# Kernel tuning notes

Measured on AMD Instinct MI355X. Metric: run time of the kernel, lower is better.

Reference implementation:

```python
import jax, jax.numpy as jnp
import numpy as np

B, L, E, H = 4, 2048, 1024, 16
D = E // H  # head_dim = 64


def setup_inputs() -> dict:
    key = jax.random.key(0)
    ks = jax.random.split(key, 8)
    s = 0.02
    return {
        "queries": jax.random.normal(ks[0], (B, L, E), jnp.float32),
        "keys": jax.random.normal(ks[1], (B, L, E), jnp.float32),
        "values": jax.random.normal(ks[2], (B, L, E), jnp.float32),
        "mask": jnp.ones((B, 1, L, L), jnp.int32),
        "Wq": jax.random.normal(ks[3], (E, E), jnp.float32) * s,
        "Wk": jax.random.normal(ks[4], (E, E), jnp.float32) * s,
        "Wv": jax.random.normal(ks[5], (E, E), jnp.float32) * s,
        "Wo": jax.random.normal(ks[6], (E, E), jnp.float32) * s,
        "bo": jax.random.normal(ks[7], (E,), jnp.float32) * s,
    }


def reference(queries, keys, values, mask, Wq, Wk, Wv, Wo, bo):
    # Linear projections (torch Linear: x @ W.T)
    q = (queries @ Wq.T).reshape(B, -1, H, D)
    k = (keys @ Wk.T).reshape(B, -1, H, D)
    v = (values @ Wv.T).reshape(B, -1, H, D)
    # scores: [B, H, Lq, Lk]
    scores = jnp.einsum("bqhd,bkhd->bhqk", q, k)
    # masked_fill BEFORE scaling, exactly as the original
    scores = jnp.where(mask == 0, jnp.float32(-1e20), scores)
    attn = jax.nn.softmax(scores / jnp.sqrt(jnp.float32(E)), axis=3)
    out = jnp.einsum("bhql,blhd->bqhd", attn, v).reshape(B, -1, H * D)
    return out @ Wo.T + bo
```

## Files before the change

### kernel.cpp

```cpp
#include <hip/hip_runtime.h>
#include <hip/hip_bf16.h>

#define B_ 4
#define L_ 2048
#define E_ 1024
#define H_ 16
#define D_ 64
#define KDIM 1024

typedef unsigned short u16;
typedef unsigned short u16x8 __attribute__((ext_vector_type(8)));
typedef short s16x8 __attribute__((ext_vector_type(8)));
typedef float f32x4 __attribute__((ext_vector_type(4)));
typedef unsigned uint2v __attribute__((ext_vector_type(2)));
typedef __fp16 h16x2 __attribute__((ext_vector_type(2)));
typedef __fp16 h16x4 __attribute__((ext_vector_type(4)));
typedef __fp16 h16x8 __attribute__((ext_vector_type(8)));

#define MFMA32(a, b, c) __builtin_amdgcn_mfma_f32_16x16x32_bf16(a, b, c, 0, 0, 0)
#define MFMA32F(a, b, c) __builtin_amdgcn_mfma_f32_16x16x32_f16(a, b, c, 0, 0, 0)

#if __has_builtin(__builtin_amdgcn_mfma_f32_16x16x16f16)
#define HAVE_F16K16 1
#define MFMA16F(a, b, c) __builtin_amdgcn_mfma_f32_16x16x16f16(a, b, c, 0, 0, 0)
#else
#define HAVE_F16K16 0
#endif

__device__ inline u16 f2bf(float f) {
  union { float f; unsigned u; } v; v.f = f;
  unsigned r = v.u + 0x7fffu + ((v.u >> 16) & 1u);
  return (u16)(r >> 16);
}
__device__ inline float bf2f(u16 h) {
  union { unsigned u; float f; } v; v.u = ((unsigned)h) << 16;
  return v.f;
}
__device__ inline float bperm_f(int byteaddr, float v) {
  return __uint_as_float((unsigned)__builtin_amdgcn_ds_bpermute(byteaddr, (int)__float_as_uint(v)));
}
__device__ inline u16 f2h_bits(float f) {
  union { __fp16 h; u16 u; } c; c.h = (__fp16)f;
  return c.u;
}

typedef __attribute__((address_space(1))) const unsigned as1_u32;
typedef __attribute__((address_space(3))) unsigned as3_u32;
__device__ inline void gl_lds16(const u16* g, u16* l) {
  __builtin_amdgcn_global_load_lds((as1_u32*)g, (as3_u32*)l, 16, 0, 0);
}

#define SCALE_Q 0.045084220f
#define MASKC  -4.508422e18f

__global__ __launch_bounds__(256) void detect_k(const u16* __restrict__ q, int* __restrict__ flag) {
  int tid = threadIdx.x;
  int cnt = 0;
  for (int i = tid; i < 4096; i += 256) {
    unsigned e = (q[i] >> 7) & 0xFFu;
    if (e >= 0xC0u) cnt++;
  }
  __shared__ int s[256];
  s[tid] = cnt;
  __syncthreads();
  for (int off = 128; off; off >>= 1) {
    if (tid < off) s[tid] += s[tid + off];
    __syncthreads();
  }
  if (tid == 0) *flag = (s[0] >= 16) ? 1 : 0;
}

__global__ __launch_bounds__(256) void mask_bits_k(const int* __restrict__ mask,
                                                   unsigned long long* __restrict__ bits,
                                                   unsigned* __restrict__ gflag, int words) {
  int gw = (int)((blockIdx.x * 256 + threadIdx.x) >> 6);
  int lane = threadIdx.x & 63;
  if (gw >= words) return;
  int mv = mask[(size_t)gw * 64 + lane];
  unsigned long long bal = __ballot(mv != 0);
  if (lane == 0) {
    bits[gw] = bal;
    if (bal != ~0ULL) atomicAnd(gflag, 0u);
  }
}

#define CH_ACT (1 << 20)
#define CH_W (1 << 17)
#define CH_TOT (128 + 3 * CH_ACT + 4 * CH_W)
__global__ __launch_bounds__(256) void cvt_all_k(
    const void* __restrict__ q, const void* __restrict__ k, const void* __restrict__ v,
    const void* __restrict__ wq, const void* __restrict__ wk, const void* __restrict__ wv,
    const void* __restrict__ wo, const void* __restrict__ bo,
    u16* __restrict__ qc, u16* __restrict__ kc, u16* __restrict__ vc,
    u16* __restrict__ wqc, u16* __restrict__ wkc, u16* __restrict__ wvc, u16* __restrict__ woc,
    float* __restrict__ bo_f, const int* __restrict__ flagp) {
  int c = blockIdx.x * 256 + threadIdx.x;
  if (c >= CH_TOT) return;
  const int isf32 = *flagp;
  if (c < 128) {
    if (isf32) {
      f32x4 a = *((const f32x4*)bo + c * 2);
      f32x4 b2 = *((const f32x4*)bo + c * 2 + 1);
      *((f32x4*)bo_f + c * 2) = a;
      *((f32x4*)bo_f + c * 2 + 1) = b2;
    } else {
      const u16* s = (const u16*)bo + c * 8;
#pragma unroll
      for (int j = 0; j < 8; ++j) bo_f[c * 8 + j] = bf2f(s[j]);
    }
    return;
  }
  if (!isf32) return;
  c -= 128;
  const void* src;
  u16* dst;
  size_t off;
  if (c < 3 * CH_ACT) {
    int t = c >> 20;
    off = (size_t)(c & (CH_ACT - 1));
    src = t == 0 ? q : (t == 1 ? k : v);
    dst = t == 0 ? qc : (t == 1 ? kc : vc);
  } else {
    int d = c - 3 * CH_ACT;
    int t = d >> 17;
    off = (size_t)(d & (CH_W - 1));
    src = t == 0 ? wq : (t == 1 ? wk : (t == 2 ? wv : wo));
    dst = t == 0 ? wqc : (t == 1 ? wkc : (t == 2 ? wvc : woc));
  }
  const float* s = (const float*)src + off * 8;
  f32x4 a = *(const f32x4*)s;
  f32x4 b2 = *(const f32x4*)(s + 4);
  u16x8 o;
#pragma unroll
  for (int j = 0; j < 4; ++j) { o[j] = f2bf(a[j]); o[4 + j] = f2bf(b2[j]); }
  *((u16x8*)dst + off) = o;
}

__device__ inline void gemm_core(const u16* __restrict__ A, const u16* __restrict__ W,
                                 int m0, int n0, u16* AsB, u16* BsB, f32x4 (&acc)[4][4]) {
  const int tid = threadIdx.x;
  const int wave = tid >> 6, lane = tid & 63;
  const int quad = lane >> 4, l16 = lane & 15;
  const int wm = wave >> 1, wn = wave & 1;
  const int lrow = lane >> 3;
  const int lch = (lane & 7) ^ lrow;

#pragma unroll
  for (int i = 0; i < 4; ++i)
#pragma unroll
    for (int j = 0; j < 4; ++j)
#pragma unroll
      for (int u = 0; u < 4; ++u) acc[i][j][u] = 0.f;

  const u16* gA = A + (size_t)(m0 + wave * 32 + lrow) * KDIM + lch * 8;
  const u16* gB = W + (size_t)(n0 + wave * 32 + lrow) * KDIM + lch * 8;

  for (int k0 = 0; k0 < KDIM; k0 += 64) {
    __syncthreads();
#pragma unroll
    for (int i = 0; i < 4; ++i) {
      gl_lds16(gA + (size_t)i * 8 * KDIM + k0, &AsB[(wave * 32 + i * 8) * 64]);
      gl_lds16(gB + (size_t)i * 8 * KDIM + k0, &BsB[(wave * 32 + i * 8) * 64]);
    }
    __syncthreads();
#pragma unroll
    for (int ks = 0; ks < 2; ++ks) {
      s16x8 af[4], bf[4];
#pragma unroll
      for (int mt = 0; mt < 4; ++mt) {
        int row = wm * 64 + mt * 16 + l16;
        af[mt] = *(const s16x8*)&AsB[row * 64 + (((quad + 4 * ks) ^ (row & 7)) * 8)];
      }
#pragma unroll
      for (int nt = 0; nt < 4; ++nt) {
        int row = wn * 64 + nt * 16 + l16;
        bf[nt] = *(const s16x8*)&BsB[row * 64 + (((quad + 4 * ks) ^ (row & 7)) * 8)];
      }
#pragma unroll
      for (int mt = 0; mt < 4; ++mt)
#pragma unroll
        for (int nt = 0; nt < 4; ++nt)
          acc[mt][nt] = MFMA32(af[mt], bf[nt], acc[mt][nt]);
    }
  }
}

__global__ __launch_bounds__(256) void gemm_proj_k(
    const void* __restrict__ qor, const void* __restrict__ kor, const void* __restrict__ vor,
    const void* __restrict__ wqor, const void* __restrict__ wkor, const void* __restrict__ wvor,
    const u16* __restrict__ qc, const u16* __restrict__ kc, const u16* __restrict__ vc,
    const u16* __restrict__ wqc, const u16* __restrict__ wkc, const u16* __restrict__ wvc,
    u16* __restrict__ Qp, u16* __restrict__ Kp, u16* __restrict__ VpT,
    const int* __restrict__ flagp) {
  const int isf32 = *flagp;
  const int z = blockIdx.z;
  __shared__ __align__(16) u16 As[128 * 64];
  __shared__ __align__(16) u16 Bs[128 * 64];
  f32x4 acc[4][4];

  const int lane = threadIdx.x & 63, wave = threadIdx.x >> 6;
  const int quad = lane >> 4, l16 = lane & 15;
  const int wm = wave >> 1, wn = wave & 1;

  if (z < 2) {
    const u16* A = z ? (isf32 ? kc : (const u16*)kor) : (isf32 ? qc : (const u16*)qor);
    const u16* W = z ? (isf32 ? wkc : (const u16*)wkor) : (isf32 ? wqc : (const u16*)wqor);
    u16* C = z ? Kp : Qp;
    const float scale = z ? 1.0f : SCALE_Q;
    const int m0 = blockIdx.y * 128, n0 = blockIdx.x * 128;
    gemm_core(A, W, m0, n0, As, Bs, acc);
#pragma unroll
    for (int mt = 0; mt < 4; ++mt)
#pragma unroll
      for (int r = 0; r < 4; ++r) {
        int row = m0 + wm * 64 + mt * 16 + quad * 4 + r;
        int bb = row >> 11, l = row & (L_ - 1);
#pragma unroll
        for (int nt = 0; nt < 4; ++nt) {
          int col = n0 + wn * 64 + nt * 16 + l16;
          int hh = col >> 6, d = col & 63;
          C[(((size_t)bb * H_ + hh) * L_ + l) * D_ + d] = f2bf(acc[mt][nt][r] * scale);
        }
      }
  } else {
    const u16* A = isf32 ? wvc : (const u16*)wvor;
    const u16* W = isf32 ? vc : (const u16*)vor;
    const int m0 = blockIdx.x * 128, n0 = blockIdx.y * 128;
    gemm_core(A, W, m0, n0, As, Bs, acc);
#pragma unroll
    for (int mt = 0; mt < 4; ++mt)
#pragma unroll
      for (int r = 0; r < 4; ++r) {
        int o = m0 + wm * 64 + mt * 16 + quad * 4 + r;
        int hh = o >> 6, d = o & 63;
#pragma unroll
        for (int nt = 0; nt < 4; ++nt) {
          int t = n0 + wn * 64 + nt * 16 + l16;
          int bb = t >> 11, l = t & (L_ - 1);
          VpT[(((size_t)bb * H_ + hh) * D_ + d) * L_ + l] = f2h_bits(acc[mt][nt][r]);
        }
      }
  }
}

__global__ __launch_bounds__(256) void gemm_out_k(
    const u16* __restrict__ AO, const void* __restrict__ woor, const u16* __restrict__ woc,
    const float* __restrict__ bo_f, void* __restrict__ outp, const int* __restrict__ flagp) {
  const int isf32 = *flagp;
  const u16* W = isf32 ? woc : (const u16*)woor;
  __shared__ __align__(16) u16 As[128 * 64];
  __shared__ __align__(16) u16 Bs[128 * 64];
  f32x4 acc[4][4];
  const int m0 = blockIdx.y * 128, n0 = blockIdx.x * 128;
  gemm_core(AO, W, m0, n0, As, Bs, acc);

  const int lane = threadIdx.x & 63, wave = threadIdx.x >> 6;
  const int quad = lane >> 4, l16 = lane & 15;
  const int wm = wave >> 1, wn = wave & 1;
#pragma unroll
  for (int mt = 0; mt < 4; ++mt)
#pragma unroll
    for (int r = 0; r < 4; ++r) {
      int row = m0 + wm * 64 + mt * 16 + quad * 4 + r;
#pragma unroll
      for (int nt = 0; nt < 4; ++nt) {
        int col = n0 + wn * 64 + nt * 16 + l16;
        float v = acc[mt][nt][r] + bo_f[col];
        if (isf32) ((float*)outp)[(size_t)row * E_ + col] = v;
        else ((u16*)outp)[(size_t)row * E_ + col] = f2bf(v);
      }
    }
}

__global__ __launch_bounds__(256) void attn_st2(
    const u16* __restrict__ Qp, const u16* __restrict__ Kp, const u16* __restrict__ VpT,
    const unsigned long long* __restrict__ Mb, const unsigned* __restrict__ allonesp,
    u16* __restrict__ AO) {
  const int qt = blockIdx.x, h = blockIdx.y, b = blockIdx.z;
  const int tid = threadIdx.x;
  const int wave = tid >> 6, lane = tid & 63;
  const int quad = lane >> 4, l16 = lane & 15;
  const size_t bh = ((size_t)b * H_ + h) * (size_t)(L_ * D_);
  const int q0w = qt * 64 + wave * 16;
  const bool aone = (*allonesp) != 0u;

  __shared__ __align__(16) u16 Ks[128 * 64];
  __shared__ __align__(16) u16 Vs[64 * 128];
#if !HAVE_F16K16
  __shared__ __align__(16) u16 Ps[4][16 * 136];
#endif

  s16x8 bq[2];
  {
    const u16* qp = &Qp[bh + (size_t)(q0w + l16) * D_ + quad * 8];
    bq[0] = *(const s16x8*)qp;
    bq[1] = *(const s16x8*)(qp + 32);
  }

  f32x4 Oacc[4];
#pragma unroll
  for (int nt = 0; nt < 4; ++nt)
#pragma unroll
    for (int u = 0; u < 4; ++u) Oacc[nt][u] = 0.f;
  float m_i = -3.0e38f, l_i = 0.f;

  const int lrow = lane >> 3, lch = (lane & 7) ^ lrow;
  const int vd_sub = lane >> 4;
  const int vchp = lane & 15;

  for (int kt = 0; kt < L_ / 128; ++kt) {
    const int k0 = kt * 128;
    __syncthreads();
#pragma unroll
    for (int i = 0; i < 4; ++i) {
      int krow = (wave * 4 + i) * 8 + lrow;
      gl_lds16(&Kp[bh + (size_t)(k0 + krow) * D_ + lch * 8], &Ks[(wave * 4 + i) * 512]);
    }
#pragma unroll
    for (int i = 0; i < 4; ++i) {
      int d = wave * 16 + i * 4 + vd_sub;
      int c = vchp ^ (i * 4 + vd_sub);
      gl_lds16(&VpT[bh + (size_t)d * L_ + k0 + c * 8], &Vs[(wave * 16 + i * 4) * 128]);
    }
    __syncthreads();

    float s[8][4];
#pragma unroll
    for (int h2 = 0; h2 < 2; ++h2)
#pragma unroll
      for (int nt = 0; nt < 4; ++nt) {
        f32x4 a = {0.f, 0.f, 0.f, 0.f};
        int row = h2 * 64 + nt * 16 + l16;
#pragma unroll
        for (int ks = 0; ks < 2; ++ks) {
          s16x8 ak = *(const s16x8*)&Ks[row * 64 + (((quad + 4 * ks) ^ (row & 7)) * 8)];
          a = MFMA32(ak, bq[ks], a);
        }
#pragma unroll
        for (int r = 0; r < 4; ++r) s[h2 * 4 + nt][r] = a[r];
      }

    if (!aone) {
      const unsigned long long* mrow = &Mb[((size_t)b * L_ + q0w + l16) * (L_ / 64) + kt * 2];
      unsigned long long mb0 = mrow[0] >> (quad * 4);
      unsigned long long mb1 = mrow[1] >> (quad * 4);
#pragma unroll
      for (int h2 = 0; h2 < 2; ++h2) {
        unsigned long long mb = h2 ? mb1 : mb0;
#pragma unroll
        for (int nt = 0; nt < 4; ++nt)
#pragma unroll
          for (int r = 0; r < 4; ++r)
            if (!((mb >> (nt * 16 + r)) & 1ULL)) s[h2 * 4 + nt][r] = MASKC;
      }
    }

    float mx = s[0][0];
#pragma unroll
    for (int knt = 0; knt < 8; ++knt)
#pragma unroll
      for (int r = 0; r < 4; ++r) mx = fmaxf(mx, s[knt][r]);
    mx = fmaxf(mx, __shfl_xor(mx, 16));
    mx = fmaxf(mx, __shfl_xor(mx, 32));
    float newm = fmaxf(m_i, mx);
    float alpha = __builtin_amdgcn_exp2f(m_i - newm);

    float rs = 0.f;
#pragma unroll
    for (int knt = 0; knt < 8; ++knt) {
      float t0 = 0.f;
#pragma unroll
      for (int r = 0; r < 4; ++r) {
        float e = __builtin_amdgcn_exp2f(s[knt][r] - newm);
        s[knt][r] = e;
        t0 += e;
      }
      rs += t0;
    }
    rs += __shfl_xor(rs, 16);
    rs += __shfl_xor(rs, 32);
    l_i = l_i * alpha + rs;
    m_i = newm;

#pragma unroll
    for (int r = 0; r < 4; ++r) {
      float aO = bperm_f((quad * 4 + r) * 4, alpha);
      Oacc[0][r] *= aO; Oacc[1][r] *= aO; Oacc[2][r] *= aO; Oacc[3][r] *= aO;
    }

#if HAVE_F16K16
#pragma unroll
    for (int knt = 0; knt < 8; ++knt) {
      union { h16x2 h2[2]; h16x4 v4; } pu;
      pu.h2[0] = __builtin_amdgcn_cvt_pkrtz(s[knt][0], s[knt][1]);
      pu.h2[1] = __builtin_amdgcn_cvt_pkrtz(s[knt][2], s[knt][3]);
      const int cbase = knt * 2 + (quad >> 1);
      const int sub = (quad & 1) * 4;
#pragma unroll
      for (int nt = 0; nt < 4; ++nt) {
        int d = nt * 16 + l16;
        const __fp16* vp = (const __fp16*)&Vs[d * 128 + ((cbase ^ (d & 15)) * 8) + sub];
        Oacc[nt] = MFMA16F(pu.v4, *(const h16x4*)vp, Oacc[nt]);
      }
    }
#else
#pragma unroll
    for (int knt = 0; knt < 8; ++knt) {
      union { h16x2 h2[2]; uint2v u; } pu;
      pu.h2[0] = __builtin_amdgcn_cvt_pkrtz(s[knt][0], s[knt][1]);
      pu.h2[1] = __builtin_amdgcn_cvt_pkrtz(s[knt][2], s[knt][3]);
      *(uint2v*)&Ps[wave][l16 * 136 + knt * 16 + quad * 4] = pu.u;
    }
#pragma unroll
    for (int ks = 0; ks < 4; ++ks) {
      h16x8 pa = *(const h16x8*)&Ps[wave][l16 * 136 + ks * 32 + quad * 8];
#pragma unroll
      for (int nt = 0; nt < 4; ++nt) {
        int d = nt * 16 + l16;
        int c = (ks * 4 + quad) ^ (d & 15);
        h16x8 vb = *(const h16x8*)&Vs[d * 128 + c * 8];
        Oacc[nt] = MFMA32F(pa, vb, Oacc[nt]);
      }
    }
#endif
  }

#pragma unroll
  for (int r = 0; r < 4; ++r) {
    float lr = bperm_f((quad * 4 + r) * 4, l_i);
    float inv = 1.0f / lr;
    int row = q0w + quad * 4 + r;
#pragma unroll
    for (int nt = 0; nt < 4; ++nt) {
      int col = h * 64 + nt * 16 + l16;
      AO[((size_t)b * L_ + row) * E_ + col] = f2bf(Oacc[nt][r] * inv);
    }
  }
}

__device__ inline u16x8 load8_cvt(const void* base, size_t elem_off, int isf32) {
  if (isf32) {
    const float* p = (const float*)base + elem_off;
    f32x4 lo = *(const f32x4*)p;
    f32x4 hi = *(const f32x4*)(p + 4);
    u16x8 t;
#pragma unroll
    for (int j = 0; j < 4; ++j) { t[j] = f2bf(lo[j]); t[4 + j] = f2bf(hi[j]); }
    return t;
  } else {
    return *((const u16x8*)base + elem_off / 8);
  }
}

template <int QKV>
__global__ __launch_bounds__(256) void gemm128(
    const void* __restrict__ A0, const void* __restrict__ A1, const void* __restrict__ A2,
    const void* __restrict__ W0, const void* __restrict__ W1, const void* __restrict__ W2,
    const void* __restrict__ bias,
    void* __restrict__ C0, u16* __restrict__ C1, u16* __restrict__ C2,
    int M, int N, int Kd, const int* __restrict__ flagp) {
  const void* A = A0; const void* W = W0; void* C = C0;
  if (QKV) {
    if (blockIdx.z == 1) { A = A1; W = W1; C = C1; }
    else if (blockIdx.z == 2) { A = A2; W = W2; C = C2; }
  }
  const int isf32 = *flagp;
  const int aF32 = QKV ? isf32 : 0;
  const int tid = threadIdx.x;
  const int wave = tid >> 6, lane = tid & 63;
  const int quad = lane >> 4, l16 = lane & 15;
  const int wm = wave >> 1, wn = wave & 1;
  const int m0 = blockIdx.y * 128, n0 = blockIdx.x * 128;
  __shared__ u16 As[128 * 32];
  __shared__ u16 Bs[128 * 32];
  f32x4 acc[4][4];
#pragma unroll
  for (int i = 0; i < 4; ++i)
#pragma unroll
    for (int j = 0; j < 4; ++j)
#pragma unroll
      for (int u = 0; u < 4; ++u) acc[i][j][u] = 0.f;
  const int row_s = tid >> 2;
  const int cb_s = tid & 3;
  for (int k0 = 0; k0 < Kd; k0 += 32) {
    __syncthreads();
#pragma unroll
    for (int rr = 0; rr < 2; ++rr) {
      int row = rr * 64 + row_s;
      int sw = (cb_s ^ ((row >> 1) & 3)) * 8;
      *(u16x8*)&As[row * 32 + sw] = load8_cvt(A, (size_t)(m0 + row) * Kd + k0 + cb_s * 8, aF32);
      *(u16x8*)&Bs[row * 32 + sw] = load8_cvt(W, (size_t)(n0 + row) * Kd + k0 + cb_s * 8, isf32);
    }
    __syncthreads();
    s16x8 af[4], bfv[4];
#pragma unroll
    for (int mt = 0; mt < 4; ++mt) {
      int row = wm * 64 + mt * 16 + l16;
      af[mt] = *(const s16x8*)&As[row * 32 + (quad ^ ((row >> 1) & 3)) * 8];
    }
#pragma unroll
    for (int nt = 0; nt < 4; ++nt) {
      int row = wn * 64 + nt * 16 + l16;
      bfv[nt] = *(const s16x8*)&Bs[row * 32 + (quad ^ ((row >> 1) & 3)) * 8];
    }
#pragma unroll
    for (int mt = 0; mt < 4; ++mt)
#pragma unroll
      for (int nt = 0; nt < 4; ++nt)
        acc[mt][nt] = MFMA32(af[mt], bfv[nt], acc[mt][nt]);
  }
#pragma unroll
  for (int mt = 0; mt < 4; ++mt)
#pragma unroll
    for (int r = 0; r < 4; ++r) {
      int row = m0 + wm * 64 + mt * 16 + quad * 4 + r;
#pragma unroll
      for (int nt = 0; nt < 4; ++nt) {
        int col = n0 + wn * 64 + nt * 16 + l16;
        float v = acc[mt][nt][r];
        if (!QKV) {
          v += isf32 ? ((const float*)bias)[col] : bf2f(((const u16*)bias)[col]);
          if (isf32) ((float*)C)[(size_t)row * N + col] = v;
          else ((u16*)C)[(size_t)row * N + col] = f2bf(v);
        } else {
          int bb = row >> 11, l = row & (L_ - 1);
          int hh = col >> 6, d = col & 63;
          ((u16*)C)[(((size_t)bb * H_ + hh) * L_ + l) * D_ + d] = f2bf(v);
        }
      }
    }
}

__global__ __launch_bounds__(256) void attn64(const u16* __restrict__ Qp, const u16* __restrict__ Kp,
                                              const u16* __restrict__ Vp,
                                              const unsigned long long* __restrict__ Mb,
                                              u16* __restrict__ AO) {
  const int qt = blockIdx.x, h = blockIdx.y, b = blockIdx.z;
  const int tid = threadIdx.x;
  const int wave = tid >> 6, lane = tid & 63;
  const int quad = lane >> 4, l16 = lane & 15;
  const size_t bh = ((size_t)b * H_ + h) * (size_t)(L_ * D_);
  const int q0 = qt * 64;
  __shared__ u16 Ksl[64 * 72];
  __shared__ u16 Vtl[64 * 72];
  __shared__ u16 Psl[4][16 * 72];
  s16x8 aq[2];
  {
    int qrow = q0 + wave * 16 + l16;
#pragma unroll
    for (int ks = 0; ks < 2; ++ks)
      aq[ks] = *(const s16x8*)&Qp[bh + (size_t)qrow * D_ + quad * 8 + 32 * ks];
  }
  f32x4 Oacc[4];
#pragma unroll
  for (int nt = 0; nt < 4; ++nt)
#pragma unroll
    for (int u = 0; u < 4; ++u) Oacc[nt][u] = 0.f;
  float m_i[4], l_i[4];
#pragma unroll
  for (int r = 0; r < 4; ++r) { m_i[r] = -3.0e38f; l_i[r] = 0.f; }
  const float invs = 0.03125f;
  const float LOG2E = 1.44269504088896f;
  for (int kt = 0; kt < L_ / 64; ++kt) {
    const int k0 = kt * 64;
    __syncthreads();
#pragma unroll
    for (int rr = 0; rr < 2; ++rr) {
      int row = rr * 32 + (tid >> 3);
      int col = (tid & 7) * 8;
      *(u16x8*)&Ksl[row * 72 + col] = *(const u16x8*)&Kp[bh + (size_t)(k0 + row) * D_ + col];
    }
    {
      int d0 = wave * 16;
#pragma unroll
      for (int half = 0; half < 2; ++half) {
        u16x8 tv = *(const u16x8*)&Vp[bh + (size_t)(k0 + lane) * D_ + d0 + half * 8];
#pragma unroll
        for (int j = 0; j < 8; ++j) Vtl[(d0 + half * 8 + j) * 72 + lane] = tv[j];
      }
    }
    __syncthreads();
    f32x4 sacc[4];
#pragma unroll
    for (int nt = 0; nt < 4; ++nt) {
#pragma unroll
      for (int u = 0; u < 4; ++u) sacc[nt][u] = 0.f;
#pragma unroll
      for (int ks = 0; ks < 2; ++ks) {
        s16x8 bfr = *(const s16x8*)&Ksl[(nt * 16 + l16) * 72 + quad * 8 + 32 * ks];
        sacc[nt] = MFMA32(aq[ks], bfr, sacc[nt]);
      }
    }
    float sv[4][4], alph[4];
#pragma unroll
    for (int r = 0; r < 4; ++r) {
      int row = q0 + wave * 16 + quad * 4 + r;
      unsigned long long mb = Mb[(size_t)(b * L_ + row) * (L_ / 64) + kt];
#pragma unroll
      for (int nt = 0; nt < 4; ++nt) {
        float s = sacc[nt][r] * invs;
        if (!((mb >> (nt * 16 + l16)) & 1ULL)) s = -3.125e18f;
        sv[nt][r] = s;
      }
      float mx = fmaxf(fmaxf(sv[0][r], sv[1][r]), fmaxf(sv[2][r], sv[3][r]));
      mx = fmaxf(mx, __shfl_xor(mx, 1));
      mx = fmaxf(mx, __shfl_xor(mx, 2));
      mx = fmaxf(mx, __shfl_xor(mx, 4));
      mx = fmaxf(mx, __shfl_xor(mx, 8));
      float newm = fmaxf(m_i[r], mx);
      float alpha = exp2f((m_i[r] - newm) * LOG2E);
      float rs = 0.f;
#pragma unroll
      for (int nt = 0; nt < 4; ++nt) {
        float pp = exp2f((sv[nt][r] - newm) * LOG2E);
        rs += pp;
        Psl[wave][(quad * 4 + r) * 72 + nt * 16 + l16] = f2bf(pp);
      }
      rs += __shfl_xor(rs, 1);
      rs += __shfl_xor(rs, 2);
      rs += __shfl_xor(rs, 4);
      rs += __shfl_xor(rs, 8);
      l_i[r] = l_i[r] * alpha + rs;
      m_i[r] = newm;
      alph[r] = alpha;
    }
#pragma unroll
    for (int nt = 0; nt < 4; ++nt)
#pragma unroll
      for (int r = 0; r < 4; ++r) Oacc[nt][r] *= alph[r];
#pragma unroll
    for (int ks = 0; ks < 2; ++ks) {
      s16x8 pa = *(const s16x8*)&Psl[wave][l16 * 72 + quad * 8 + 32 * ks];
#pragma unroll
      for (int nt = 0; nt < 4; ++nt) {
        s16x8 vb = *(const s16x8*)&Vtl[(nt * 16 + l16) * 72 + quad * 8 + 32 * ks];
        Oacc[nt] = MFMA32(pa, vb, Oacc[nt]);
      }
    }
  }
#pragma unroll
  for (int nt = 0; nt < 4; ++nt)
#pragma unroll
    for (int r = 0; r < 4; ++r) {
      int row = q0 + wave * 16 + quad * 4 + r;
      int col = h * 64 + nt * 16 + l16;
      AO[((size_t)b * L_ + row) * E_ + col] = f2bf(Oacc[nt][r] / l_i[r]);
    }
}

extern "C" void kernel_launch(void* const* d_in, const int* in_sizes, int n_in,
                              void* d_out, int out_size, void* d_ws, size_t ws_size,
                              hipStream_t stream) {
  const void* queries = d_in[0];
  const void* keys = d_in[1];
  const void* values = d_in[2];
  const int* mask = (const int*)d_in[3];
  const void* Wq = d_in[4];
  const void* Wk = d_in[5];
  const void* Wv = d_in[6];
  const void* Wo = d_in[7];
  const void* bo = d_in[8];

  char* ws = (char*)d_ws;
  const int words = B_ * L_ * (L_ / 64);
  const size_t NEED = 111153408;

  if (ws_size >= NEED) {
    const size_t SZQ = (size_t)B_ * L_ * E_ * 2;
    const size_t SZW = (size_t)E_ * E_ * 2;
    u16* qc = (u16*)(ws + 0);
    u16* kc = (u16*)(ws + SZQ);
    u16* vc = (u16*)(ws + 2 * SZQ);
    u16* wqc = (u16*)(ws + 3 * SZQ);
    u16* wkc = (u16*)(ws + 3 * SZQ + SZW);
    u16* wvc = (u16*)(ws + 3 * SZQ + 2 * SZW);
    u16* woc = (u16*)(ws + 3 * SZQ + 3 * SZW);
    float* bo_f = (float*)(ws + 3 * SZQ + 4 * SZW);
    char* p2 = ws + 3 * SZQ + 4 * SZW + 4096;
    u16* Qp = (u16*)(p2);
    u16* Kp = (u16*)(p2 + SZQ);
    u16* VpT = (u16*)(p2 + 2 * SZQ);
    unsigned long long* Mb = (unsigned long long*)(p2 + 3 * SZQ);
    char* pf = p2 + 3 * SZQ + (size_t)words * 8;
    int* flag = (int*)pf;
    unsigned* gflag = (unsigned*)(pf + 4);
    u16* AO = qc;

    hipLaunchKernelGGL(detect_k, dim3(1), dim3(256), 0, stream, (const u16*)queries, flag);
    (void)hipMemsetAsync(gflag, 1, 4, stream);
    hipLaunchKernelGGL(mask_bits_k, dim3(words / 4), dim3(256), 0, stream, mask, Mb, gflag, words);
    hipLaunchKernelGGL(cvt_all_k, dim3((CH_TOT + 255) / 256), dim3(256), 0, stream,
                       queries, keys, values, Wq, Wk, Wv, Wo, bo,
                       qc, kc, vc, wqc, wkc, wvc, woc, bo_f, flag);
    hipLaunchKernelGGL(gemm_proj_k, dim3(E_ / 128, (B_ * L_) / 128, 3), dim3(256), 0, stream,
                       queries, keys, values, Wq, Wk, Wv,
                       qc, kc, vc, wqc, wkc, wvc, Qp, Kp, VpT, flag);
    hipLaunchKernelGGL(attn_st2, dim3(L_ / 64, H_, B_), dim3(256), 0, stream,
                       Qp, Kp, VpT, Mb, gflag, AO);
    hipLaunchKernelGGL(gemm_out_k, dim3(E_ / 128, (B_ * L_) / 128, 1), dim3(256), 0, stream,
                       AO, Wo, woc, bo_f, d_out, flag);
  } else {
    const size_t SEG = (size_t)B_ * H_ * L_ * D_ * sizeof(u16);
    u16* Qp = (u16*)(ws);
    u16* Kp = (u16*)(ws + SEG);
    u16* Vp = (u16*)(ws + 2 * SEG);
    u16* AO = (u16*)(ws + 3 * SEG);
    int* flag = (int*)(ws + 4 * SEG);
    unsigned* gflag = (unsigned*)(ws + 4 * SEG + 8);
    unsigned long long* Mb = (unsigned long long*)(ws + 4 * SEG + 256);

    hipLaunchKernelGGL(detect_k, dim3(1), dim3(256), 0, stream, (const u16*)queries, flag);
    (void)hipMemsetAsync(gflag, 1, 4, stream);
    hipLaunchKernelGGL(mask_bits_k, dim3(words / 4), dim3(256), 0, stream, mask, Mb, gflag, words);
    dim3 g1(E_ / 128, (B_ * L_) / 128, 3);
    hipLaunchKernelGGL((gemm128<1>), g1, dim3(256), 0, stream,
                       queries, keys, values, Wq, Wk, Wv, (const void*)nullptr,
                       (void*)Qp, Kp, Vp, B_ * L_, E_, E_, flag);
    hipLaunchKernelGGL(attn64, dim3(L_ / 64, H_, B_), dim3(256), 0, stream, Qp, Kp, Vp, Mb, AO);
    dim3 g2(E_ / 128, (B_ * L_) / 128, 1);
    hipLaunchKernelGGL((gemm128<0>), g2, dim3(256), 0, stream,
                       (const void*)AO, (const void*)nullptr, (const void*)nullptr,
                       Wo, (const void*)nullptr, (const void*)nullptr, bo,
                       d_out, (u16*)nullptr, (u16*)nullptr, B_ * L_, E_, E_, flag);
  }
}
```

Before: 444.5 us.

## Fuse mask packing into conversion kernel and compute softmax row sums via MFMA

Merges the mask-bit packing kernel and the dtype-conversion kernel into one launch, removing one kernel launch and its tail. In attention, the softmax denominator is now accumulated with an extra MFMA against a ones vector instead of per-lane adds plus cross-lane shuffles. The rescale of the output accumulators is skipped when no lane's running max grew. The max reduction is rewritten as a tree. Accumulating the row sum from fp16-rounded probabilities slightly changes numerics and adds one MFMA per step.

```diff
diff --git a/kernel.cpp b/kernel.cpp
--- a/kernel.cpp
+++ b/kernel.cpp
@@ -70,31 +70,35 @@
   if (tid == 0) *flag = (s[0] >= 16) ? 1 : 0;
 }
 
-__global__ __launch_bounds__(256) void mask_bits_k(const int* __restrict__ mask,
-                                                   unsigned long long* __restrict__ bits,
-                                                   unsigned* __restrict__ gflag, int words) {
-  int gw = (int)((blockIdx.x * 256 + threadIdx.x) >> 6);
-  int lane = threadIdx.x & 63;
-  if (gw >= words) return;
-  int mv = mask[(size_t)gw * 64 + lane];
-  unsigned long long bal = __ballot(mv != 0);
-  if (lane == 0) {
-    bits[gw] = bal;
-    if (bal != ~0ULL) atomicAnd(gflag, 0u);
-  }
-}
-
 #define CH_ACT (1 << 20)
 #define CH_W (1 << 17)
 #define CH_TOT (128 + 3 * CH_ACT + 4 * CH_W)
-__global__ __launch_bounds__(256) void cvt_all_k(
+#define MBLK ((B_ * L_ * (L_ / 64)) / 4)
+#define CVB ((CH_TOT + 255) / 256)
+
+__global__ __launch_bounds__(256) void prep_k(
+    const int* __restrict__ mask, unsigned long long* __restrict__ bits,
+    unsigned* __restrict__ gflag,
     const void* __restrict__ q, const void* __restrict__ k, const void* __restrict__ v,
     const void* __restrict__ wq, const void* __restrict__ wk, const void* __restrict__ wv,
     const void* __restrict__ wo, const void* __restrict__ bo,
     u16* __restrict__ qc, u16* __restrict__ kc, u16* __restrict__ vc,
     u16* __restrict__ wqc, u16* __restrict__ wkc, u16* __restrict__ wvc, u16* __restrict__ woc,
     float* __restrict__ bo_f, const int* __restrict__ flagp) {
-  int c = blockIdx.x * 256 + threadIdx.x;
+  int bid = blockIdx.x;
+  int tid = threadIdx.x;
+  if (bid < MBLK) {
+    int gw = (bid * 256 + tid) >> 6;
+    int lane = tid & 63;
+    int mv = mask[(size_t)gw * 64 + lane];
+    unsigned long long bal = __ballot(mv != 0);
+    if (lane == 0) {
+      bits[gw] = bal;
+      if (bal != ~0ULL) atomicAnd(gflag, 0u);
+    }
+    return;
+  }
+  int c = (bid - MBLK) * 256 + tid;
   if (c >= CH_TOT) return;
   const int isf32 = *flagp;
   if (c < 128) {
@@ -272,7 +276,7 @@
     }
 }
 
-__global__ __launch_bounds__(256) void attn_st2(
+__global__ __launch_bounds__(256) void attn_st3(
     const u16* __restrict__ Qp, const u16* __restrict__ Kp, const u16* __restrict__ VpT,
     const unsigned long long* __restrict__ Mb, const unsigned* __restrict__ allonesp,
     u16* __restrict__ AO) {
@@ -298,11 +302,16 @@
   }
 
   f32x4 Oacc[4];
+  f32x4 Racc;
 #pragma unroll
   for (int nt = 0; nt < 4; ++nt)
 #pragma unroll
     for (int u = 0; u < 4; ++u) Oacc[nt][u] = 0.f;
-  float m_i = -3.0e38f, l_i = 0.f;
+#pragma unroll
+  for (int u = 0; u < 4; ++u) Racc[u] = 0.f;
+  float m_i = -3.0e38f;
+
+  const h16x4 onesb = {(__fp16)1.f, (__fp16)1.f, (__fp16)1.f, (__fp16)1.f};
 
   const int lrow = lane >> 3, lch = (lane & 7) ^ lrow;
   const int vd_sub = lane >> 4;
@@ -355,38 +364,47 @@
       }
     }
 
-    float mx = s[0][0];
-#pragma unroll
-    for (int knt = 0; knt < 8; ++knt)
-#pragma unroll
-      for (int r = 0; r < 4; ++r) mx = fmaxf(mx, s[knt][r]);
+    float mx;
+    {
+      float t0 = fmaxf(fmaxf(s[0][0], s[0][1]), s[0][2]);
+      float t1 = fmaxf(fmaxf(s[0][3], s[1][0]), s[1][1]);
+      float t2 = fmaxf(fmaxf(s[1][2], s[1][3]), s[2][0]);
+      float t3 = fmaxf(fmaxf(s[2][1], s[2][2]), s[2][3]);
+      float t4 = fmaxf(fmaxf(s[3][0], s[3][1]), s[3][2]);
+      float t5 = fmaxf(fmaxf(s[3][3], s[4][0]), s[4][1]);
+      float t6 = fmaxf(fmaxf(s[4][2], s[4][3]), s[5][0]);
+      float t7 = fmaxf(fmaxf(s[5][1], s[5][2]), s[5][3]);
+      float t8 = fmaxf(fmaxf(s[6][0], s[6][1]), s[6][2]);
+      float t9 = fmaxf(fmaxf(s[6][3], s[7][0]), s[7][1]);
+      float ta = fmaxf(s[7][2], s[7][3]);
+      float u0 = fmaxf(fmaxf(t0, t1), t2);
+      float u1 = fmaxf(fmaxf(t3, t4), t5);
+      float u2 = fmaxf(fmaxf(t6, t7), t8);
+      float u3 = fmaxf(t9, ta);
+      mx = fmaxf(fmaxf(u0, u1), fmaxf(u2, u3));
+    }
     mx = fmaxf(mx, __shfl_xor(mx, 16));
     mx = fmaxf(mx, __shfl_xor(mx, 32));
-    float newm = fmaxf(m_i, mx);
-    float alpha = __builtin_amdgcn_exp2f(m_i - newm);
-
-    float rs = 0.f;
-#pragma unroll
-    for (int knt = 0; knt < 8; ++knt) {
-      float t0 = 0.f;
+
+    const float oldm = m_i;
+    const float newm = fmaxf(oldm, mx);
+    m_i = newm;
+
+    if (__ballot(newm > oldm)) {
+      float alpha = __builtin_amdgcn_exp2f(oldm - newm);
 #pragma unroll
       for (int r = 0; r < 4; ++r) {
-        float e = __builtin_amdgcn_exp2f(s[knt][r] - newm);
-        s[knt][r] = e;
-        t0 += e;
-      }
-      rs += t0;
-    }
-    rs += __shfl_xor(rs, 16);
-    rs += __shfl_xor(rs, 32);
-    l_i = l_i * alpha + rs;
-    m_i = newm;
-
-#pragma unroll
-    for (int r = 0; r < 4; ++r) {
-      float aO = bperm_f((quad * 4 + r) * 4, alpha);
-      Oacc[0][r] *= aO; Oacc[1][r] *= aO; Oacc[2][r] *= aO; Oacc[3][r] *= aO;
-    }
+        float aO = bperm_f((quad * 4 + r) * 4, alpha);
+        Oacc[0][r] *= aO; Oacc[1][r] *= aO; Oacc[2][r] *= aO; Oacc[3][r] *= aO;
+        Racc[r] *= aO;
+      }
+    }
+
+#pragma unroll
+    for (int knt = 0; knt < 8; ++knt)
+#pragma unroll
+      for (int r = 0; r < 4; ++r)
+        s[knt][r] = __builtin_amdgcn_exp2f(s[knt][r] - newm);
 
 #if HAVE_F16K16
 #pragma unroll
@@ -402,6 +420,7 @@
         const __fp16* vp = (const __fp16*)&Vs[d * 128 + ((cbase ^ (d & 15)) * 8) + sub];
         Oacc[nt] = MFMA16F(pu.v4, *(const h16x4*)vp, Oacc[nt]);
       }
+      Racc = MFMA16F(pu.v4, onesb, Racc);
     }
 #else
 #pragma unroll
@@ -411,6 +430,8 @@
       pu.h2[1] = __builtin_amdgcn_cvt_pkrtz(s[knt][2], s[knt][3]);
       *(uint2v*)&Ps[wave][l16 * 136 + knt * 16 + quad * 4] = pu.u;
     }
+    const h16x8 ones8 = {(__fp16)1.f, (__fp16)1.f, (__fp16)1.f, (__fp16)1.f,
+                         (__fp16)1.f, (__fp16)1.f, (__fp16)1.f, (__fp16)1.f};
 #pragma unroll
     for (int ks = 0; ks < 4; ++ks) {
       h16x8 pa = *(const h16x8*)&Ps[wave][l16 * 136 + ks * 32 + quad * 8];
@@ -421,20 +442,34 @@
         h16x8 vb = *(const h16x8*)&Vs[d * 128 + c * 8];
         Oacc[nt] = MFMA32F(pa, vb, Oacc[nt]);
       }
+      Racc = MFMA32F(pa, ones8, Racc);
     }
 #endif
   }
 
 #pragma unroll
   for (int r = 0; r < 4; ++r) {
-    float lr = bperm_f((quad * 4 + r) * 4, l_i);
-    float inv = 1.0f / lr;
+    float inv = 1.0f / Racc[r];
     int row = q0w + quad * 4 + r;
 #pragma unroll
     for (int nt = 0; nt < 4; ++nt) {
       int col = h * 64 + nt * 16 + l16;
       AO[((size_t)b * L_ + row) * E_ + col] = f2bf(Oacc[nt][r] * inv);
     }
+  }
+}
+
+__global__ __launch_bounds__(256) void mask_bits_k(const int* __restrict__ mask,
+                                                   unsigned long long* __restrict__ bits,
+                                                   unsigned* __restrict__ gflag, int words) {
+  int gw = (int)((blockIdx.x * 256 + threadIdx.x) >> 6);
+  int lane = threadIdx.x & 63;
+  if (gw >= words) return;
+  int mv = mask[(size_t)gw * 64 + lane];
+  unsigned long long bal = __ballot(mv != 0);
+  if (lane == 0) {
+    bits[gw] = bal;
+    if (bal != ~0ULL) atomicAnd(gflag, 0u);
   }
 }
 
@@ -688,14 +723,14 @@
 
     hipLaunchKernelGGL(detect_k, dim3(1), dim3(256), 0, stream, (const u16*)queries, flag);
     (void)hipMemsetAsync(gflag, 1, 4, stream);
-    hipLaunchKernelGGL(mask_bits_k, dim3(words / 4), dim3(256), 0, stream, mask, Mb, gflag, words);
-    hipLaunchKernelGGL(cvt_all_k, dim3((CH_TOT + 255) / 256), dim3(256), 0, stream,
+    hipLaunchKernelGGL(prep_k, dim3(MBLK + CVB), dim3(256), 0, stream,
+                       mask, Mb, gflag,
                        queries, keys, values, Wq, Wk, Wv, Wo, bo,
                        qc, kc, vc, wqc, wkc, wvc, woc, bo_f, flag);
     hipLaunchKernelGGL(gemm_proj_k, dim3(E_ / 128, (B_ * L_) / 128, 3), dim3(256), 0, stream,
                        queries, keys, values, Wq, Wk, Wv,
                        qc, kc, vc, wqc, wkc, wvc, Qp, Kp, VpT, flag);
-    hipLaunchKernelGGL(attn_st2, dim3(L_ / 64, H_, B_), dim3(256), 0, stream,
+    hipLaunchKernelGGL(attn_st3, dim3(L_ / 64, H_, B_), dim3(256), 0, stream,
                        Qp, Kp, VpT, Mb, gflag, AO);
     hipLaunchKernelGGL(gemm_out_k, dim3(E_ / 128, (B_ * L_) / 128, 1), dim3(256), 0, stream,
                        AO, Wo, woc, bo_f, d_out, flag);
```

After: 441.7 us. About the same (-0.6%).
